# Performance work log

Hardware: AMD Instinct MI355X
Metric: run time of the kernel (lower is better)

## Reference

```python
import jax, jax.numpy as jnp
import numpy as np

D = 768      # hidden_dim
H = 8        # num_heads
K = 5        # k_neighbors
L = 3        # num_layers
EPS = 1e-5   # LayerNorm eps (torch default)


def _layernorm(x, g, b):
    mu = jnp.mean(x, axis=-1, keepdims=True)
    var = jnp.mean((x - mu) ** 2, axis=-1, keepdims=True)
    return (x - mu) * jax.lax.rsqrt(var + EPS) * g + b


def setup_inputs() -> dict:
    key = jax.random.key(0)
    B, S = 8, 1024
    ks = jax.random.split(key, 16)
    s = 0.02
    inp = {
        "x": jax.random.normal(ks[0], (B, S, D), dtype=jnp.float32),
        # per-layer stacked params (leading axis L=3)
        "gcn_w": jax.random.normal(ks[1], (L, D, D), dtype=jnp.float32) * s,
        "gcn_b": jnp.zeros((L, D), dtype=jnp.float32),
        "attn_in_w": jax.random.normal(ks[2], (L, 3 * D, D), dtype=jnp.float32) * s,
        "attn_in_b": jnp.zeros((L, 3 * D), dtype=jnp.float32),
        "attn_out_w": jax.random.normal(ks[3], (L, D, D), dtype=jnp.float32) * s,
        "attn_out_b": jnp.zeros((L, D), dtype=jnp.float32),
        "ln_g": jnp.ones((L, D), dtype=jnp.float32),
        "ln_b": jnp.zeros((L, D), dtype=jnp.float32),
        "gate_w": jax.random.normal(ks[4], (L, D, 2 * D), dtype=jnp.float32) * s,
        "gate_b": jnp.zeros((L, D), dtype=jnp.float32),
        "proj_w": jax.random.normal(ks[5], (D, D), dtype=jnp.float32) * s,
        "proj_b": jnp.zeros((D,), dtype=jnp.float32),
    }
    return inp


def reference(x, gcn_w, gcn_b, attn_in_w, attn_in_b, attn_out_w, attn_out_b,
              ln_g, ln_b, gate_w, gate_b, proj_w, proj_b):
    B, S, _ = x.shape
    dh = D // H

    # ---- DynamicGraphConstructor: per-batch kNN graph, symmetrized + deduped.
    # Dense boolean adjacency is the exact equivalent of the unique'd edge list.
    sim = jnp.einsum('bsd,btd->bst', x, x)                 # [B,S,S]
    topk_idx = jax.lax.top_k(sim, K)[1]                    # [B,S,K]
    bi = jnp.arange(B)[:, None, None]
    si = jnp.arange(S)[None, :, None]
    A = jnp.zeros((B, S, S), dtype=bool).at[bi, si, topk_idx].set(True)
    A = A | jnp.swapaxes(A, 1, 2)                          # bidirectional edges
    A = A | jnp.eye(S, dtype=bool)                         # GCN self-loops (add_remaining)
    Af = A.astype(x.dtype)
    deg = jnp.sum(Af, axis=-1)                             # [B,S], >= 1
    dinv = jax.lax.rsqrt(deg)
    An = Af * dinv[:, :, None] * dinv[:, None, :]          # D^-1/2 (A+I) D^-1/2

    scale = 1.0 / float(np.sqrt(dh))
    h = x                                                  # [B,S,D]
    for l in range(L):
        # GCNConv: norm-adj aggregation of linearly transformed features + bias
        gcn = jnp.einsum('bst,btd->bsd', An, h @ gcn_w[l].T) + gcn_b[l]

        # nn.MultiheadAttention (packed qkv in-proj, scaled dot-product, out-proj)
        qkv = h @ attn_in_w[l].T + attn_in_b[l]            # [B,S,3D]
        q, k, v = jnp.split(qkv, 3, axis=-1)
        q = q.reshape(B, S, H, dh).transpose(0, 2, 1, 3)   # [B,H,S,dh]
        k = k.reshape(B, S, H, dh).transpose(0, 2, 1, 3)
        v = v.reshape(B, S, H, dh).transpose(0, 2, 1, 3)
        scores = jnp.einsum('bhsd,bhtd->bhst', q, k) * scale
        attn = jax.nn.softmax(scores, axis=-1)
        ao = jnp.einsum('bhst,bhtd->bhsd', attn, v)
        ao = ao.transpose(0, 2, 1, 3).reshape(B, S, D)
        ao = ao @ attn_out_w[l].T + attn_out_b[l]

        # learned fusion gate + residual + LayerNorm (norm1 is unused upstream)
        gate = jax.nn.sigmoid(
            jnp.concatenate([gcn, ao], axis=-1) @ gate_w[l].T + gate_b[l])
        fused = gate * gcn + (1.0 - gate) * ao
        h = _layernorm(fused + h, ln_g[l], ln_b[l])

    return h @ proj_w.T + proj_b
```

## Files before the change

### kernel.cpp

```cpp
#include <hip/hip_runtime.h>
#include <hip/hip_bf16.h>
#include <math.h>

using bf16 = __hip_bfloat16;

#define B_  8
#define S_  1024
#define D_  768
#define H_  8
#define DH_ 96
#define TD_ 2304
#define L_  3
#define GK_ 1536
#define NC_ 3072
#define MAXE_ 98304

typedef __attribute__((ext_vector_type(8))) short short8v;
typedef __attribute__((ext_vector_type(4))) float f32x4;

static inline size_t align_up(size_t x) { return (x + 255) & ~(size_t)255; }

__device__ inline short bfbits(float f) {
    unsigned x = __float_as_uint(f);
    unsigned r = (x + 0x7fffu + ((x >> 16) & 1u)) >> 16;
    return (short)r;
}
__device__ inline float bf2f(const bf16 s) { return __bfloat162float(s); }

__global__ __launch_bounds__(256)
void gemm_f32_bt_k(const float* __restrict__ X, long long xbs, int ldx,
                   const float* __restrict__ W, long long wbs, int ldw,
                   float* __restrict__ C, long long cbs, int ldc, int K)
{
    const int gx = gridDim.x, gy = gridDim.y;
    int flat = blockIdx.x + gx * (blockIdx.y + gy * blockIdx.z);
    const int nwg = gx * gy * gridDim.z;
    const int cpx = nwg >> 3;
    flat = (flat & 7) * cpx + (flat >> 3);
    const int bx = flat % gx;
    const int by = (flat / gx) % gy;
    const int bz = flat / (gx * gy);

    __shared__ float As[16][132];
    __shared__ float Bs[16][68];
    X += (long long)bz * xbs;
    W += (long long)bz * wbs;
    C += (long long)bz * cbs;
    const int tid = threadIdx.x;
    const int tx = tid & 15, ty = tid >> 4;
    const int m0 = by * 128, n0 = bx * 64;
    float acc[8][4] = {};
    for (int k0 = 0; k0 < K; k0 += 16) {
#pragma unroll
        for (int it = 0; it < 2; ++it) {
            int c = tid + it * 256;
            int row = c >> 2, jq = c & 3;
            float4 v = *(const float4*)&X[(long long)(m0 + row) * ldx + k0 + jq * 4];
            As[jq * 4 + 0][row] = v.x; As[jq * 4 + 1][row] = v.y;
            As[jq * 4 + 2][row] = v.z; As[jq * 4 + 3][row] = v.w;
        }
        {
            int row = tid >> 2, jq = tid & 3;
            float4 v = *(const float4*)&W[(long long)(n0 + row) * ldw + k0 + jq * 4];
            Bs[jq * 4 + 0][row] = v.x; Bs[jq * 4 + 1][row] = v.y;
            Bs[jq * 4 + 2][row] = v.z; Bs[jq * 4 + 3][row] = v.w;
        }
        __syncthreads();
#pragma unroll
        for (int kk = 0; kk < 16; ++kk) {
            float4 a0 = *(const float4*)&As[kk][ty * 4];
            float4 a1 = *(const float4*)&As[kk][64 + ty * 4];
            float4 b0 = *(const float4*)&Bs[kk][tx * 4];
            float a[8] = {a0.x, a0.y, a0.z, a0.w, a1.x, a1.y, a1.z, a1.w};
            float b[4] = {b0.x, b0.y, b0.z, b0.w};
#pragma unroll
            for (int i = 0; i < 8; ++i)
#pragma unroll
                for (int j = 0; j < 4; ++j)
                    acc[i][j] = fmaf(a[i], b[j], acc[i][j]);
        }
        __syncthreads();
    }
#pragma unroll
    for (int ih = 0; ih < 2; ++ih)
#pragma unroll
        for (int i = 0; i < 4; ++i) {
            int row = m0 + ih * 64 + ty * 4 + i;
            float4 v = make_float4(acc[ih * 4 + i][0], acc[ih * 4 + i][1],
                                   acc[ih * 4 + i][2], acc[ih * 4 + i][3]);
            *(float4*)&C[(long long)row * ldc + n0 + tx * 4] = v;
        }
}

template<int OUTMODE>
__global__ __launch_bounds__(256)
void mfma_gemm_k(const bf16* __restrict__ X, int ldx,
                 const bf16* __restrict__ W, int ldw,
                 float* __restrict__ C, int ldc,
                 bf16* __restrict__ Cb, int ldcb,
                 bf16* __restrict__ Cb2, int ldcb2, int ncut,
                 const float* __restrict__ bias, int K)
{
    __shared__ short As[128 * 32];
    __shared__ short Bs[128 * 32];
    const int tid = threadIdx.x;
    const int l = tid & 63;
    const int w = tid >> 6;
    const int wm = w >> 1, wn = w & 1;
    const int m0 = blockIdx.y * 128, n0 = blockIdx.x * 128;

    const int frow = l & 15;
    const int koff = (l >> 4) * 8;

    f32x4 acc[4][4] = {};

    for (int k0 = 0; k0 < K; k0 += 32) {
        __syncthreads();
#pragma unroll
        for (int it = 0; it < 2; ++it) {
            int c = it * 256 + tid;
            const bf16* ga = X + (long long)(m0 + (c >> 2)) * ldx + k0 + (c & 3) * 8;
            __builtin_amdgcn_global_load_lds(
                (const __attribute__((address_space(1))) void*)ga,
                (__attribute__((address_space(3))) void*)&As[c * 8], 16, 0, 0);
            const bf16* gb = W + (long long)(n0 + (c >> 2)) * ldw + k0 + (c & 3) * 8;
            __builtin_amdgcn_global_load_lds(
                (const __attribute__((address_space(1))) void*)gb,
                (__attribute__((address_space(3))) void*)&Bs[c * 8], 16, 0, 0);
        }
        __syncthreads();

        short8v a[4], b[4];
#pragma unroll
        for (int mi = 0; mi < 4; ++mi)
            a[mi] = *(const short8v*)&As[(wm * 64 + mi * 16 + frow) * 32 + koff];
#pragma unroll
        for (int ni = 0; ni < 4; ++ni)
            b[ni] = *(const short8v*)&Bs[(wn * 64 + ni * 16 + frow) * 32 + koff];
        __builtin_amdgcn_s_setprio(1);
#pragma unroll
        for (int mi = 0; mi < 4; ++mi)
#pragma unroll
            for (int ni = 0; ni < 4; ++ni)
                acc[mi][ni] = __builtin_amdgcn_mfma_f32_16x16x32_bf16(
                    a[mi], b[ni], acc[mi][ni], 0, 0, 0);
        __builtin_amdgcn_s_setprio(0);
    }

    const int rbase = (l >> 4) * 4;
    const int ccol = l & 15;
    const bool second = (OUTMODE == 3) && (n0 >= ncut);
#pragma unroll
    for (int mi = 0; mi < 4; ++mi) {
#pragma unroll
        for (int ni = 0; ni < 4; ++ni) {
            int col = n0 + wn * 64 + ni * 16 + ccol;
            float bv = 0.0f;
            if (OUTMODE != 3) { if (bias) bv = bias[col]; }
            else if (second)  { bv = bias[col - ncut]; }
#pragma unroll
            for (int j = 0; j < 4; ++j) {
                int row = m0 + wm * 64 + mi * 16 + rbase + j;
                float v = acc[mi][ni][j] + bv;
                if (OUTMODE == 0) {
                    C[(long long)row * ldc + col] = v;
                } else if (OUTMODE == 2) {
                    Cb[(long long)row * ldcb + col] = __float2bfloat16(v);
                } else {
                    if (second)
                        Cb2[(long long)row * ldcb2 + (col - ncut)] = __float2bfloat16(v);
                    else
                        Cb[(long long)row * ldcb + col] = __float2bfloat16(v);
                }
            }
        }
    }
}

__global__ void cvt_bf_k(const float* __restrict__ src, bf16* __restrict__ dst, long long n)
{
    long long stride = (long long)gridDim.x * blockDim.x;
    for (long long i = (long long)blockIdx.x * blockDim.x + threadIdx.x; i * 8 < n; i += stride) {
        float4 v0 = ((const float4*)src)[i * 2];
        float4 v1 = ((const float4*)src)[i * 2 + 1];
        short8v o;
        o[0] = bfbits(v0.x); o[1] = bfbits(v0.y); o[2] = bfbits(v0.z); o[3] = bfbits(v0.w);
        o[4] = bfbits(v1.x); o[5] = bfbits(v1.y); o[6] = bfbits(v1.z); o[7] = bfbits(v1.w);
        *(short8v*)&dst[i * 8] = o;
    }
}

__global__ void cvt_wcat_k(const float* __restrict__ gw, const float* __restrict__ aiw,
                           bf16* __restrict__ wcat)
{
    const long long nch = (long long)L_ * NC_ * D_ / 8;
    long long stride = (long long)gridDim.x * blockDim.x;
    for (long long i = (long long)blockIdx.x * blockDim.x + threadIdx.x; i < nch; i += stride) {
        long long e8 = i * 8;
        int l = (int)(e8 / ((long long)NC_ * D_));
        long long rem = e8 - (long long)l * NC_ * D_;
        int n = (int)(rem / D_);
        int k = (int)(rem - (long long)n * D_);
        const float* src = (n < D_)
            ? gw  + ((size_t)l * D_  + n)        * D_ + k
            : aiw + ((size_t)l * TD_ + (n - D_)) * D_ + k;
        float4 v0 = *(const float4*)src;
        float4 v1 = *(const float4*)(src + 4);
        short8v o;
        o[0] = bfbits(v0.x); o[1] = bfbits(v0.y); o[2] = bfbits(v0.z); o[3] = bfbits(v0.w);
        o[4] = bfbits(v1.x); o[5] = bfbits(v1.y); o[6] = bfbits(v1.z); o[7] = bfbits(v1.w);
        *(short8v*)&wcat[e8] = o;
    }
}

__global__ void zero32_k(unsigned int* __restrict__ p, long long n32)
{
    for (long long i = (long long)blockIdx.x * blockDim.x + threadIdx.x; i < n32;
         i += (long long)gridDim.x * blockDim.x)
        p[i] = 0u;
}

__global__ __launch_bounds__(256)
void topk_k(const float* __restrict__ sim, int* __restrict__ idx)
{
    const int r = blockIdx.x * 4 + (threadIdx.x >> 6);
    const int lane = threadIdx.x & 63;
    const float* row = sim + (long long)r * S_;
    const float NEG = -3.4e38f;
    float v0 = NEG, v1 = NEG, v2 = NEG, v3 = NEG, v4 = NEG;
    int i0 = -1, i1 = -1, i2 = -1, i3 = -1, i4 = -1;
#pragma unroll
    for (int j = 0; j < 16; ++j) {
        int t = lane + j * 64;
        float xv = row[t];
        if (xv > v4) {
            v4 = xv; i4 = t;
            if (v4 > v3) { float tv = v3; v3 = v4; v4 = tv; int ti = i3; i3 = i4; i4 = ti; }
            if (v3 > v2) { float tv = v2; v2 = v3; v3 = tv; int ti = i2; i2 = i3; i3 = ti; }
            if (v2 > v1) { float tv = v1; v1 = v2; v2 = tv; int ti = i1; i1 = i2; i2 = ti; }
            if (v1 > v0) { float tv = v0; v0 = v1; v1 = tv; int ti = i0; i0 = i1; i1 = ti; }
        }
    }
    int o0, o1, o2, o3, o4;
#pragma unroll
    for (int round = 0; round < 5; ++round) {
        float bv = v0; int bi = i0;
        if (v1 > bv || (v1 == bv && i1 < bi)) { bv = v1; bi = i1; }
        if (v2 > bv || (v2 == bv && i2 < bi)) { bv = v2; bi = i2; }
        if (v3 > bv || (v3 == bv && i3 < bi)) { bv = v3; bi = i3; }
        if (v4 > bv || (v4 == bv && i4 < bi)) { bv = v4; bi = i4; }
#pragma unroll
        for (int off = 1; off < 64; off <<= 1) {
            float ov = __shfl_xor(bv, off, 64);
            int oi = __shfl_xor(bi, off, 64);
            if (ov > bv || (ov == bv && oi < bi)) { bv = ov; bi = oi; }
        }
        if (i0 == bi) v0 = NEG;
        else if (i1 == bi) v1 = NEG;
        else if (i2 == bi) v2 = NEG;
        else if (i3 == bi) v3 = NEG;
        else if (i4 == bi) v4 = NEG;
        if (round == 0) o0 = bi;
        else if (round == 1) o1 = bi;
        else if (round == 2) o2 = bi;
        else if (round == 3) o3 = bi;
        else o4 = bi;
    }
    if (lane == 0) {
        idx[r * 5 + 0] = o0; idx[r * 5 + 1] = o1; idx[r * 5 + 2] = o2;
        idx[r * 5 + 3] = o3; idx[r * 5 + 4] = o4;
    }
}

__global__ void adj_k(const int* __restrict__ idx, unsigned char* __restrict__ adj)
{
    int r = blockIdx.x * blockDim.x + threadIdx.x;
    if (r >= B_ * S_) return;
    int b = r >> 10, s = r & (S_ - 1);
    unsigned char* Ab = adj + (long long)b * S_ * S_;
    Ab[(long long)s * S_ + s] = 1;
    for (int j = 0; j < 5; ++j) {
        int t = idx[r * 5 + j];
        Ab[(long long)s * S_ + t] = 1;
        Ab[(long long)t * S_ + s] = 1;
    }
}

__global__ void deg_dinv_k(const unsigned char* __restrict__ adj,
                           int* __restrict__ deg, float* __restrict__ dinv)
{
    int r = blockIdx.x * blockDim.x + threadIdx.x;
    if (r >= B_ * S_) return;
    const unsigned int* row = (const unsigned int*)(adj + (long long)r * S_);
    int dsum = 0;
    for (int t = 0; t < S_ / 4; ++t)
        dsum += __popc(row[t]);
    deg[r] = dsum;
    dinv[r] = rsqrtf((float)dsum);
}

__global__ __launch_bounds__(1024)
void scan_k(const int* __restrict__ deg, int* __restrict__ off)
{
    __shared__ int buf[1024];
    const int tid = threadIdx.x;
    int loc[8];
    int s = 0;
#pragma unroll
    for (int i = 0; i < 8; ++i) { loc[i] = deg[tid * 8 + i]; s += loc[i]; }
    buf[tid] = s;
    __syncthreads();
    for (int d = 1; d < 1024; d <<= 1) {
        int v = (tid >= d) ? buf[tid - d] : 0;
        __syncthreads();
        buf[tid] += v;
        __syncthreads();
    }
    int base = buf[tid] - s;
#pragma unroll
    for (int i = 0; i < 8; ++i) { off[tid * 8 + i] = base; base += loc[i]; }
    if (tid == 1023) off[B_ * S_] = buf[1023];
}

__global__ __launch_bounds__(256)
void csr_fill_k(const unsigned char* __restrict__ adj, const float* __restrict__ dinv,
                const int* __restrict__ off, int* __restrict__ nidx,
                float* __restrict__ nwt)
{
    const int r = blockIdx.x * 4 + (threadIdx.x >> 6);
    const int lane = threadIdx.x & 63;
    const int b = r >> 10;
    const unsigned int* row = (const unsigned int*)(adj + (long long)r * S_);
    unsigned int w0 = row[lane * 4 + 0], w1 = row[lane * 4 + 1];
    unsigned int w2 = row[lane * 4 + 2], w3 = row[lane * 4 + 3];
    int cnt = __popc(w0) + __popc(w1) + __popc(w2) + __popc(w3);
    int pre = cnt;
#pragma unroll
    for (int d = 1; d < 64; d <<= 1) {
        int v = __shfl_up(pre, d, 64);
        if (lane >= d) pre += v;
    }
    int p = off[r] + pre - cnt;
    const float dr = dinv[r];
#pragma unroll
    for (int q = 0; q < 16; ++q) {
        unsigned int word = (q < 4) ? w0 : (q < 8) ? w1 : (q < 12) ? w2 : w3;
        if ((word >> (8 * (q & 3))) & 0xffu) {
            int t = lane * 16 + q;
            nidx[p] = t;
            nwt[p] = dr * dinv[(b << 10) + t];
            ++p;
        }
    }
}

__global__ __launch_bounds__(256)
void gcn_agg_k(const int* __restrict__ off, const int* __restrict__ nidx,
               const float* __restrict__ nwt, const bf16* __restrict__ Y,
               const float* __restrict__ gb, bf16* __restrict__ cat)
{
    const int bid = blockIdx.x;
    const int r = (bid & 7) * 1024 + (bid >> 3);
    const int tid = threadIdx.x;
    const long long rowbase = (long long)(r & ~(S_ - 1)) * D_;
    const int s = off[r], e = off[r + 1];
    float a0 = 0.f, a1 = 0.f, a2 = 0.f;
    for (int p = s; p < e; ++p) {
        int t = nidx[p];
        float wt = nwt[p];
        const bf16* yr = Y + rowbase + (long long)t * D_;
        a0 = fmaf(wt, bf2f(yr[tid]), a0);
        a1 = fmaf(wt, bf2f(yr[tid + 256]), a1);
        a2 = fmaf(wt, bf2f(yr[tid + 512]), a2);
    }
    long long cbase = (long long)r * GK_;
    cat[cbase + tid]       = __float2bfloat16(a0 + gb[tid]);
    cat[cbase + tid + 256] = __float2bfloat16(a1 + gb[tid + 256]);
    cat[cbase + tid + 512] = __float2bfloat16(a2 + gb[tid + 512]);
}

__global__ __launch_bounds__(256)
void flash_k(const bf16* __restrict__ qkv, bf16* __restrict__ ao)
{
    const int q0 = blockIdx.x * 128;
    const int bh = blockIdx.y;
    const int b = bh >> 3, h = bh & 7;
    const int tid = threadIdx.x;
    const int w = tid >> 6;
    const int l = tid & 63;
    const float scale = 0.10206207261596575f;

    __shared__ short Ks[64][104];
    __shared__ short Vt[96][72];
    __shared__ short Ps[4][32][72];

    const int frow = l & 15;
    const int koff = (l >> 4) * 8;

    short8v qfA[3], qfB[3];
    {
        const bf16* qa = qkv + ((long long)b * S_ + q0 + w * 32 + frow) * TD_ + h * DH_ + koff;
        const bf16* qb = qa + 16 * TD_;
#pragma unroll
        for (int kc = 0; kc < 3; ++kc) {
            qfA[kc] = *(const short8v*)(qa + kc * 32);
            qfB[kc] = *(const short8v*)(qb + kc * 32);
        }
    }

    float psA[4] = {0.f, 0.f, 0.f, 0.f}, psB[4] = {0.f, 0.f, 0.f, 0.f};
    f32x4 OA[6] = {}, OB[6] = {};

    for (int t0 = 0; t0 < S_; t0 += 64) {
        __syncthreads();
        const bf16* kb = qkv + ((long long)b * S_ + t0) * TD_ + D_ + h * DH_;
        const bf16* vb = kb + D_;
        for (int c = tid; c < 768; c += 256) {
            int row = c / 12, c8 = c % 12;
            *(short8v*)&Ks[row][c8 * 8] =
                *(const short8v*)(kb + (long long)row * TD_ + c8 * 8);
        }
        for (int c = tid; c < 768; c += 256) {
            int row = c & 63, c8 = c >> 6;
            short8v vv = *(const short8v*)(vb + (long long)row * TD_ + c8 * 8);
#pragma unroll
            for (int j = 0; j < 8; ++j)
                Vt[c8 * 8 + j][row] = vv[j];
        }
        __syncthreads();

        {
            f32x4 s[2][4] = {};
            __builtin_amdgcn_s_setprio(1);
#pragma unroll
            for (int kc = 0; kc < 3; ++kc) {
#pragma unroll
                for (int ni = 0; ni < 4; ++ni) {
                    short8v kf = *(const short8v*)&Ks[ni * 16 + frow][kc * 32 + koff];
                    s[0][ni] = __builtin_amdgcn_mfma_f32_16x16x32_bf16(qfA[kc], kf, s[0][ni], 0, 0, 0);
                    s[1][ni] = __builtin_amdgcn_mfma_f32_16x16x32_bf16(qfB[kc], kf, s[1][ni], 0, 0, 0);
                }
            }
            __builtin_amdgcn_s_setprio(0);
            int crow = (l >> 4) * 4;
            int ccol = l & 15;
#pragma unroll
            for (int ni = 0; ni < 4; ++ni) {
#pragma unroll
                for (int j = 0; j < 4; ++j) {
                    float pA = __expf(s[0][ni][j] * scale);
                    float pB = __expf(s[1][ni][j] * scale);
                    Ps[w][crow + j][ni * 16 + ccol]      = bfbits(pA);
                    Ps[w][16 + crow + j][ni * 16 + ccol] = bfbits(pB);
                    psA[j] += pA;
                    psB[j] += pB;
                }
            }
        }

        {
            short8v paA0 = *(const short8v*)&Ps[w][frow][koff];
            short8v paA1 = *(const short8v*)&Ps[w][frow][32 + koff];
            short8v paB0 = *(const short8v*)&Ps[w][16 + frow][koff];
            short8v paB1 = *(const short8v*)&Ps[w][16 + frow][32 + koff];
            __builtin_amdgcn_s_setprio(1);
#pragma unroll
            for (int dt = 0; dt < 6; ++dt) {
                short8v bf0 = *(const short8v*)&Vt[dt * 16 + frow][koff];
                short8v bf1 = *(const short8v*)&Vt[dt * 16 + frow][32 + koff];
                OA[dt] = __builtin_amdgcn_mfma_f32_16x16x32_bf16(paA0, bf0, OA[dt], 0, 0, 0);
                OA[dt] = __builtin_amdgcn_mfma_f32_16x16x32_bf16(paA1, bf1, OA[dt], 0, 0, 0);
                OB[dt] = __builtin_amdgcn_mfma_f32_16x16x32_bf16(paB0, bf0, OB[dt], 0, 0, 0);
                OB[dt] = __builtin_amdgcn_mfma_f32_16x16x32_bf16(paB1, bf1, OB[dt], 0, 0, 0);
            }
            __builtin_amdgcn_s_setprio(0);
        }
    }

    float invA[4], invB[4];
#pragma unroll
    for (int j = 0; j < 4; ++j) {
        float sA = psA[j], sB = psB[j];
#pragma unroll
        for (int msk = 1; msk < 16; msk <<= 1) {
            sA += __shfl_xor(sA, msk, 64);
            sB += __shfl_xor(sB, msk, 64);
        }
        invA[j] = 1.0f / sA;
        invB[j] = 1.0f / sB;
    }

#pragma unroll
    for (int dt = 0; dt < 6; ++dt) {
#pragma unroll
        for (int j = 0; j < 4; ++j) {
            int rowA = q0 + w * 32 + (l >> 4) * 4 + j;
            int col = h * DH_ + dt * 16 + (l & 15);
            ao[((long long)b * S_ + rowA) * D_ + col] = __float2bfloat16(OA[dt][j] * invA[j]);
            ao[((long long)b * S_ + rowA + 16) * D_ + col] = __float2bfloat16(OB[dt][j] * invB[j]);
        }
    }
}

__global__ __launch_bounds__(256)
void fuse_ln_k(const bf16* __restrict__ gbuf, const bf16* __restrict__ cat,
               bf16* __restrict__ h_bf,
               const float* __restrict__ lng, const float* __restrict__ lnb)
{
    const int r = blockIdx.x;
    const int tid = threadIdx.x;
    const long long base = (long long)r * D_;
    const long long cbase = (long long)r * GK_;
    __shared__ float rs1[4], rs2[4];

    float tv[3];
    float s1 = 0.f, s2 = 0.f;
#pragma unroll
    for (int q = 0; q < 3; ++q) {
        int j = tid + q * 256;
        float g = 1.0f / (1.0f + expf(-bf2f(gbuf[base + j])));
        float gc = bf2f(cat[cbase + j]);
        float av = bf2f(cat[cbase + D_ + j]);
        float t = g * gc + (1.0f - g) * av + bf2f(h_bf[base + j]);
        tv[q] = t;
        s1 += t;
        s2 += t * t;
    }
#pragma unroll
    for (int off = 32; off; off >>= 1) {
        s1 += __shfl_down(s1, off, 64);
        s2 += __shfl_down(s2, off, 64);
    }
    if ((tid & 63) == 0) { rs1[tid >> 6] = s1; rs2[tid >> 6] = s2; }
    __syncthreads();
    float S1 = rs1[0] + rs1[1] + rs1[2] + rs1[3];
    float S2 = rs2[0] + rs2[1] + rs2[2] + rs2[3];
    float mu = S1 * (1.0f / D_);
    float var = S2 * (1.0f / D_) - mu * mu;
    float rinv = rsqrtf(var + 1e-5f);
#pragma unroll
    for (int q = 0; q < 3; ++q) {
        int j = tid + q * 256;
        float v = (tv[q] - mu) * rinv * lng[j] + lnb[j];
        h_bf[base + j] = __float2bfloat16(v);
    }
}

extern "C" void kernel_launch(void* const* d_in, const int* in_sizes, int n_in,
                              void* d_out, int out_size, void* d_ws, size_t ws_size,
                              hipStream_t stream)
{
    (void)in_sizes; (void)n_in; (void)out_size;
    const float* x          = (const float*)d_in[0];
    const float* gcn_w      = (const float*)d_in[1];
    const float* gcn_b      = (const float*)d_in[2];
    const float* attn_in_w  = (const float*)d_in[3];
    const float* attn_in_b  = (const float*)d_in[4];
    const float* attn_out_w = (const float*)d_in[5];
    const float* attn_out_b = (const float*)d_in[6];
    const float* ln_g       = (const float*)d_in[7];
    const float* ln_b       = (const float*)d_in[8];
    const float* gate_w     = (const float*)d_in[9];
    const float* gate_b     = (const float*)d_in[10];
    const float* proj_w     = (const float*)d_in[11];
    const float* proj_b     = (const float*)d_in[12];
    float* out = (float*)d_out;

    char* ws = (char*)d_ws;
    size_t off = 0;
    auto alloc = [&](size_t bytes) { void* p = ws + off; off = align_up(off + bytes); return p; };
    const size_t nBSD = (size_t)B_ * S_ * D_;
    bf16*  h_bf  = (bf16*)alloc(nBSD * 2);
    float* sim   = (float*)alloc((size_t)B_ * S_ * S_ * 4);
    bf16*  gbuf  = (bf16*)sim;
    bf16*  Y_bf  = (bf16*)alloc(nBSD * 2);
    bf16*  cat   = (bf16*)alloc((size_t)B_ * S_ * GK_ * 2);
    bf16*  qkv_bf= (bf16*)alloc((size_t)B_ * S_ * TD_ * 2);
    bf16*  ao_bf = (bf16*)alloc(nBSD * 2);
    unsigned char* adj = (unsigned char*)alloc((size_t)B_ * S_ * S_);
    float* dinv  = (float*)alloc((size_t)B_ * S_ * 4);
    int*   deg   = (int*)alloc((size_t)B_ * S_ * 4);
    int*   offs  = (int*)alloc(((size_t)B_ * S_ + 1) * 4);
    int*   nidx  = (int*)alloc((size_t)MAXE_ * 4);
    float* nwt   = (float*)alloc((size_t)MAXE_ * 4);
    int*   tki   = (int*)alloc((size_t)B_ * S_ * 5 * 4);
    bf16* wcat   = (bf16*)alloc((size_t)L_ * NC_ * D_ * 2);
    bf16* aow_bf = (bf16*)alloc((size_t)L_ * D_ * D_ * 2);
    bf16* gtw_bf = (bf16*)alloc((size_t)L_ * D_ * 2 * D_ * 2);
    bf16* pw_bf  = (bf16*)alloc((size_t)D_ * D_ * 2);
    if (off > ws_size) return;

    cvt_bf_k<<<1024, 256, 0, stream>>>(x, h_bf, nBSD);
    cvt_wcat_k<<<2048, 256, 0, stream>>>(gcn_w, attn_in_w, wcat);
    cvt_bf_k<<<1024, 256, 0, stream>>>(attn_out_w, aow_bf, (long long)L_ * D_ * D_);
    cvt_bf_k<<<1024, 256, 0, stream>>>(gate_w, gtw_bf, (long long)L_ * D_ * 2 * D_);
    cvt_bf_k<<<256, 256, 0, stream>>>(proj_w, pw_bf, (long long)D_ * D_);

    {
        dim3 g(S_ / 64, S_ / 128, B_);
        gemm_f32_bt_k<<<g, 256, 0, stream>>>(
            x, (long long)S_ * D_, D_, x, (long long)S_ * D_, D_,
            sim, (long long)S_ * S_, S_, D_);
    }
    topk_k<<<B_ * S_ / 4, 256, 0, stream>>>(sim, tki);
    zero32_k<<<2048, 256, 0, stream>>>((unsigned int*)adj, (long long)B_ * S_ * S_ / 4);
    adj_k<<<(B_ * S_ + 255) / 256, 256, 0, stream>>>(tki, adj);
    deg_dinv_k<<<(B_ * S_ + 255) / 256, 256, 0, stream>>>(adj, deg, dinv);
    scan_k<<<1, 1024, 0, stream>>>(deg, offs);
    csr_fill_k<<<B_ * S_ / 4, 256, 0, stream>>>(adj, dinv, offs, nidx, nwt);

    dim3 gD(D_ / 128, (B_ * S_) / 128);
    dim3 gNC(NC_ / 128, (B_ * S_) / 128);
    for (int l = 0; l < L_; ++l) {
        const bf16* wc  = wcat + (size_t)l * NC_ * D_;
        const bf16* aow = aow_bf + (size_t)l * D_ * D_;
        const bf16* gtw = gtw_bf + (size_t)l * D_ * 2 * D_;

        mfma_gemm_k<3><<<gNC, 256, 0, stream>>>(
            h_bf, D_, wc, D_, nullptr, 0, Y_bf, D_, qkv_bf, TD_, D_,
            attn_in_b + l * TD_, D_);
        gcn_agg_k<<<B_ * S_, 256, 0, stream>>>(offs, nidx, nwt, Y_bf, gcn_b + l * D_, cat);
        {
            dim3 g(S_ / 128, B_ * H_);
            flash_k<<<g, 256, 0, stream>>>(qkv_bf, ao_bf);
        }
        mfma_gemm_k<2><<<gD, 256, 0, stream>>>(
            ao_bf, D_, aow, D_, nullptr, 0, cat + D_, GK_, nullptr, 0, 0,
            attn_out_b + l * D_, D_);
        mfma_gemm_k<2><<<gD, 256, 0, stream>>>(
            cat, GK_, gtw, GK_, nullptr, 0, gbuf, D_, nullptr, 0, 0,
            gate_b + l * D_, GK_);
        fuse_ln_k<<<B_ * S_, 256, 0, stream>>>(gbuf, cat, h_bf,
                                               ln_g + l * D_, ln_b + l * D_);
    }

    mfma_gemm_k<0><<<gD, 256, 0, stream>>>(
        h_bf, D_, pw_bf, D_, out, D_, nullptr, 0, nullptr, 0, 0, proj_b, D_);
}
```

Before: 910.9 us.

## Prefetch next tiles in sim GEMM and flash attention, shrink M tile for narrow GEMMs

The fp32 similarity GEMM and the flash-attention kernel now load the next K/V (or A/B) tile into registers while computing on the current shared-memory tile, aiming to hide global-memory latency. The MFMA GEMM gains an M-tile template parameter, and the D-wide GEMMs use 64-row tiles so that more workgroups are launched for these 768-column outputs. The GCN aggregation loop gets an unroll hint. The prefetching costs more registers and an extra barrier per iteration, which may lower occupancy.

```diff
diff --git a/kernel.cpp b/kernel.cpp
--- a/kernel.cpp
+++ b/kernel.cpp
@@ -49,23 +49,41 @@
     const int tid = threadIdx.x;
     const int tx = tid & 15, ty = tid >> 4;
     const int m0 = by * 128, n0 = bx * 64;
+
+    const int ar0 = tid >> 2,            aj0 = tid & 3;
+    const int ar1 = (tid + 256) >> 2,    aj1 = tid & 3;
+    const int br  = tid >> 2,            bj  = tid & 3;
+
+    auto ldA = [&](int k0, int row, int jq) {
+        return *(const float4*)&X[(long long)(m0 + row) * ldx + k0 + jq * 4];
+    };
+    auto ldB = [&](int k0, int row, int jq) {
+        return *(const float4*)&W[(long long)(n0 + row) * ldw + k0 + jq * 4];
+    };
+    auto stage = [&](float4 a0, float4 a1, float4 b) {
+        As[aj0 * 4 + 0][ar0] = a0.x; As[aj0 * 4 + 1][ar0] = a0.y;
+        As[aj0 * 4 + 2][ar0] = a0.z; As[aj0 * 4 + 3][ar0] = a0.w;
+        As[aj1 * 4 + 0][ar1] = a1.x; As[aj1 * 4 + 1][ar1] = a1.y;
+        As[aj1 * 4 + 2][ar1] = a1.z; As[aj1 * 4 + 3][ar1] = a1.w;
+        Bs[bj * 4 + 0][br] = b.x; Bs[bj * 4 + 1][br] = b.y;
+        Bs[bj * 4 + 2][br] = b.z; Bs[bj * 4 + 3][br] = b.w;
+    };
+
     float acc[8][4] = {};
+    {
+        float4 a0 = ldA(0, ar0, aj0), a1 = ldA(0, ar1, aj1), b = ldB(0, br, bj);
+        stage(a0, a1, b);
+    }
+    __syncthreads();
+
     for (int k0 = 0; k0 < K; k0 += 16) {
-#pragma unroll
-        for (int it = 0; it < 2; ++it) {
-            int c = tid + it * 256;
-            int row = c >> 2, jq = c & 3;
-            float4 v = *(const float4*)&X[(long long)(m0 + row) * ldx + k0 + jq * 4];
-            As[jq * 4 + 0][row] = v.x; As[jq * 4 + 1][row] = v.y;
-            As[jq * 4 + 2][row] = v.z; As[jq * 4 + 3][row] = v.w;
-        }
-        {
-            int row = tid >> 2, jq = tid & 3;
-            float4 v = *(const float4*)&W[(long long)(n0 + row) * ldw + k0 + jq * 4];
-            Bs[jq * 4 + 0][row] = v.x; Bs[jq * 4 + 1][row] = v.y;
-            Bs[jq * 4 + 2][row] = v.z; Bs[jq * 4 + 3][row] = v.w;
-        }
-        __syncthreads();
+        const bool more = (k0 + 16) < K;
+        float4 na0, na1, nb;
+        if (more) {
+            na0 = ldA(k0 + 16, ar0, aj0);
+            na1 = ldA(k0 + 16, ar1, aj1);
+            nb  = ldB(k0 + 16, br, bj);
+        }
 #pragma unroll
         for (int kk = 0; kk < 16; ++kk) {
             float4 a0 = *(const float4*)&As[kk][ty * 4];
@@ -79,7 +97,11 @@
                 for (int j = 0; j < 4; ++j)
                     acc[i][j] = fmaf(a[i], b[j], acc[i][j]);
         }
-        __syncthreads();
+        if (more) {
+            __syncthreads();
+            stage(na0, na1, nb);
+            __syncthreads();
+        }
     }
 #pragma unroll
     for (int ih = 0; ih < 2; ++ih)
@@ -92,7 +114,7 @@
         }
 }
 
-template<int OUTMODE>
+template<int OUTMODE, int MT>
 __global__ __launch_bounds__(256)
 void mfma_gemm_k(const bf16* __restrict__ X, int ldx,
                  const bf16* __restrict__ W, int ldw,
@@ -101,28 +123,34 @@
                  bf16* __restrict__ Cb2, int ldcb2, int ncut,
                  const float* __restrict__ bias, int K)
 {
-    __shared__ short As[128 * 32];
+    constexpr int MFR = MT / 32;
+    constexpr int AIT = MT / 64;
+    __shared__ short As[MT * 32];
     __shared__ short Bs[128 * 32];
     const int tid = threadIdx.x;
     const int l = tid & 63;
     const int w = tid >> 6;
     const int wm = w >> 1, wn = w & 1;
-    const int m0 = blockIdx.y * 128, n0 = blockIdx.x * 128;
+    const int m0 = blockIdx.y * MT, n0 = blockIdx.x * 128;
 
     const int frow = l & 15;
     const int koff = (l >> 4) * 8;
 
-    f32x4 acc[4][4] = {};
+    f32x4 acc[MFR][4] = {};
 
     for (int k0 = 0; k0 < K; k0 += 32) {
         __syncthreads();
 #pragma unroll
-        for (int it = 0; it < 2; ++it) {
+        for (int it = 0; it < AIT; ++it) {
             int c = it * 256 + tid;
             const bf16* ga = X + (long long)(m0 + (c >> 2)) * ldx + k0 + (c & 3) * 8;
             __builtin_amdgcn_global_load_lds(
                 (const __attribute__((address_space(1))) void*)ga,
                 (__attribute__((address_space(3))) void*)&As[c * 8], 16, 0, 0);
+        }
+#pragma unroll
+        for (int it = 0; it < 2; ++it) {
+            int c = it * 256 + tid;
             const bf16* gb = W + (long long)(n0 + (c >> 2)) * ldw + k0 + (c & 3) * 8;
             __builtin_amdgcn_global_load_lds(
                 (const __attribute__((address_space(1))) void*)gb,
@@ -130,16 +158,16 @@
         }
         __syncthreads();
 
-        short8v a[4], b[4];
-#pragma unroll
-        for (int mi = 0; mi < 4; ++mi)
-            a[mi] = *(const short8v*)&As[(wm * 64 + mi * 16 + frow) * 32 + koff];
+        short8v a[MFR], b[4];
+#pragma unroll
+        for (int mi = 0; mi < MFR; ++mi)
+            a[mi] = *(const short8v*)&As[(wm * (MT / 2) + mi * 16 + frow) * 32 + koff];
 #pragma unroll
         for (int ni = 0; ni < 4; ++ni)
             b[ni] = *(const short8v*)&Bs[(wn * 64 + ni * 16 + frow) * 32 + koff];
         __builtin_amdgcn_s_setprio(1);
 #pragma unroll
-        for (int mi = 0; mi < 4; ++mi)
+        for (int mi = 0; mi < MFR; ++mi)
 #pragma unroll
             for (int ni = 0; ni < 4; ++ni)
                 acc[mi][ni] = __builtin_amdgcn_mfma_f32_16x16x32_bf16(
@@ -151,7 +179,7 @@
     const int ccol = l & 15;
     const bool second = (OUTMODE == 3) && (n0 >= ncut);
 #pragma unroll
-    for (int mi = 0; mi < 4; ++mi) {
+    for (int mi = 0; mi < MFR; ++mi) {
 #pragma unroll
         for (int ni = 0; ni < 4; ++ni) {
             int col = n0 + wn * 64 + ni * 16 + ccol;
@@ -160,7 +188,7 @@
             else if (second)  { bv = bias[col - ncut]; }
 #pragma unroll
             for (int j = 0; j < 4; ++j) {
-                int row = m0 + wm * 64 + mi * 16 + rbase + j;
+                int row = m0 + wm * (MT / 2) + mi * 16 + rbase + j;
                 float v = acc[mi][ni][j] + bv;
                 if (OUTMODE == 0) {
                     C[(long long)row * ldc + col] = v;
@@ -365,6 +393,7 @@
     const long long rowbase = (long long)(r & ~(S_ - 1)) * D_;
     const int s = off[r], e = off[r + 1];
     float a0 = 0.f, a1 = 0.f, a2 = 0.f;
+#pragma unroll 2
     for (int p = s; p < e; ++p) {
         int t = nidx[p];
         float wt = nwt[p];
@@ -397,6 +426,14 @@
     const int frow = l & 15;
     const int koff = (l >> 4) * 8;
 
+    int krow[3], kc8[3], vrow[3], vc8[3];
+#pragma unroll
+    for (int ii = 0; ii < 3; ++ii) {
+        int c = tid + ii * 256;
+        krow[ii] = c / 12; kc8[ii] = c % 12;
+        vrow[ii] = c & 63; vc8[ii] = c >> 6;
+    }
+
     short8v qfA[3], qfB[3];
     {
         const bf16* qa = qkv + ((long long)b * S_ + q0 + w * 32 + frow) * TD_ + h * DH_ + koff;
@@ -408,26 +445,39 @@
         }
     }
 
+    auto loadKV = [&](int t0, short8v (&kr)[3], short8v (&vr)[3]) {
+        const bf16* kb = qkv + ((long long)b * S_ + t0) * TD_ + D_ + h * DH_;
+        const bf16* vb = kb + D_;
+#pragma unroll
+        for (int ii = 0; ii < 3; ++ii) {
+            kr[ii] = *(const short8v*)(kb + (long long)krow[ii] * TD_ + kc8[ii] * 8);
+            vr[ii] = *(const short8v*)(vb + (long long)vrow[ii] * TD_ + vc8[ii] * 8);
+        }
+    };
+    auto writeKV = [&](const short8v (&kr)[3], const short8v (&vr)[3]) {
+#pragma unroll
+        for (int ii = 0; ii < 3; ++ii) {
+            *(short8v*)&Ks[krow[ii]][kc8[ii] * 8] = kr[ii];
+#pragma unroll
+            for (int j = 0; j < 8; ++j)
+                Vt[vc8[ii] * 8 + j][vrow[ii]] = vr[ii][j];
+        }
+    };
+
     float psA[4] = {0.f, 0.f, 0.f, 0.f}, psB[4] = {0.f, 0.f, 0.f, 0.f};
     f32x4 OA[6] = {}, OB[6] = {};
 
+    {
+        short8v kr[3], vr[3];
+        loadKV(0, kr, vr);
+        writeKV(kr, vr);
+    }
+    __syncthreads();
+
     for (int t0 = 0; t0 < S_; t0 += 64) {
-        __syncthreads();
-        const bf16* kb = qkv + ((long long)b * S_ + t0) * TD_ + D_ + h * DH_;
-        const bf16* vb = kb + D_;
-        for (int c = tid; c < 768; c += 256) {
-            int row = c / 12, c8 = c % 12;
-            *(short8v*)&Ks[row][c8 * 8] =
-                *(const short8v*)(kb + (long long)row * TD_ + c8 * 8);
-        }
-        for (int c = tid; c < 768; c += 256) {
-            int row = c & 63, c8 = c >> 6;
-            short8v vv = *(const short8v*)(vb + (long long)row * TD_ + c8 * 8);
-#pragma unroll
-            for (int j = 0; j < 8; ++j)
-                Vt[c8 * 8 + j][row] = vv[j];
-        }
-        __syncthreads();
+        const bool more = (t0 + 64) < S_;
+        short8v nkr[3], nvr[3];
+        if (more) loadKV(t0 + 64, nkr, nvr);
 
         {
             f32x4 s[2][4] = {};
@@ -474,6 +524,12 @@
                 OB[dt] = __builtin_amdgcn_mfma_f32_16x16x32_bf16(paB1, bf1, OB[dt], 0, 0, 0);
             }
             __builtin_amdgcn_s_setprio(0);
+        }
+
+        if (more) {
+            __syncthreads();
+            writeKV(nkr, nvr);
+            __syncthreads();
         }
     }
 
@@ -609,14 +665,14 @@
     scan_k<<<1, 1024, 0, stream>>>(deg, offs);
     csr_fill_k<<<B_ * S_ / 4, 256, 0, stream>>>(adj, dinv, offs, nidx, nwt);
 
-    dim3 gD(D_ / 128, (B_ * S_) / 128);
+    dim3 gD64(D_ / 128, (B_ * S_) / 64);
     dim3 gNC(NC_ / 128, (B_ * S_) / 128);
     for (int l = 0; l < L_; ++l) {
         const bf16* wc  = wcat + (size_t)l * NC_ * D_;
         const bf16* aow = aow_bf + (size_t)l * D_ * D_;
         const bf16* gtw = gtw_bf + (size_t)l * D_ * 2 * D_;
 
-        mfma_gemm_k<3><<<gNC, 256, 0, stream>>>(
+        mfma_gemm_k<3, 128><<<gNC, 256, 0, stream>>>(
             h_bf, D_, wc, D_, nullptr, 0, Y_bf, D_, qkv_bf, TD_, D_,
             attn_in_b + l * TD_, D_);
         gcn_agg_k<<<B_ * S_, 256, 0, stream>>>(offs, nidx, nwt, Y_bf, gcn_b + l * D_, cat);
@@ -624,16 +680,16 @@
             dim3 g(S_ / 128, B_ * H_);
             flash_k<<<g, 256, 0, stream>>>(qkv_bf, ao_bf);
         }
-        mfma_gemm_k<2><<<gD, 256, 0, stream>>>(
+        mfma_gemm_k<2, 64><<<gD64, 256, 0, stream>>>(
             ao_bf, D_, aow, D_, nullptr, 0, cat + D_, GK_, nullptr, 0, 0,
             attn_out_b + l * D_, D_);
-        mfma_gemm_k<2><<<gD, 256, 0, stream>>>(
+        mfma_gemm_k<2, 64><<<gD64, 256, 0, stream>>>(
             cat, GK_, gtw, GK_, nullptr, 0, gbuf, D_, nullptr, 0, 0,
             gate_b + l * D_, GK_);
         fuse_ln_k<<<B_ * S_, 256, 0, stream>>>(gbuf, cat, h_bf,
                                                ln_g + l * D_, ln_b + l * D_);
     }
 
-    mfma_gemm_k<0><<<gD, 256, 0, stream>>>(
+    mfma_gemm_k<0, 64><<<gD64, 256, 0, stream>>>(
         h_bf, D_, pw_bf, D_, out, D_, nullptr, 0, nullptr, 0, 0, proj_b, D_);
 }
```

Result: faster. 866.3 us (-4.9%).
